# Kernel optimization log

Measured on AMD Instinct MI355X. Metric: run time of the kernel, lower is better.

Reference implementation:

```python
import jax, jax.numpy as jnp
import numpy as np

D_MODEL = 1024
NUM_HEADS = 16
B, S = 1, 4096


def setup_inputs() -> dict:
    key = jax.random.key(0)
    kx, kq, kk, kv, ko = jax.random.split(key, 5)
    std = (1.0 / D_MODEL) ** 0.5
    def trunc(k):
        return std * jax.random.truncated_normal(k, -3.0, 3.0, (D_MODEL, D_MODEL), dtype=jnp.float32)
    return {
        "x": jax.random.normal(kx, (B, S, D_MODEL), dtype=jnp.float32),
        "W_Q": trunc(kq),
        "W_K": trunc(kk),
        "W_V": trunc(kv),
        "W_O": trunc(ko),
    }


def reference(x, W_Q, W_K, W_V, W_O):
    Bx, Sx, Dm = x.shape
    H = NUM_HEADS
    d_attn = Dm // H
    # projections (torch code uses x @ W.T)
    Q = x @ W_Q.T
    K = x @ W_K.T
    V = x @ W_V.T
    # [B, H, S, d]
    Q = Q.reshape(Bx, Sx, H, d_attn).transpose(0, 2, 1, 3)
    K = K.reshape(Bx, Sx, H, d_attn).transpose(0, 2, 1, 3)
    V = V.reshape(Bx, Sx, H, d_attn).transpose(0, 2, 1, 3)
    scale = 1.0 / jnp.sqrt(jnp.asarray(d_attn, dtype=x.dtype))
    # [B, H, S, S] scores
    attn = jnp.einsum("bhqd,bhkd->bhqk", Q, K) * scale
    causal = jnp.tril(jnp.ones((Sx, Sx), dtype=bool))
    attn = jnp.where(causal, attn, jnp.asarray(-jnp.inf, dtype=attn.dtype))
    probs = jax.nn.softmax(attn, axis=-1)
    y = jnp.einsum("bhqk,bhkd->bhqd", probs, V)
    y = y.transpose(0, 2, 1, 3).reshape(Bx, Sx, Dm)
    return y @ W_O.T
```

## Files before the change

kernel.cpp:

```cpp
#include <hip/hip_runtime.h>

#define S_LEN 4096
#define DMODEL 1024
#define NHEADS 16

typedef __attribute__((ext_vector_type(8))) short bf16x8;
typedef __attribute__((ext_vector_type(4))) float f32x4;
typedef unsigned short u16;
typedef unsigned int u32;
typedef unsigned long long u64;

__device__ inline u16 f2bf(float f) {
    union { float f; u32 u; } v; v.f = f;
    u32 r = v.u + 0x7fffu + ((v.u >> 16) & 1u);
    return (u16)(r >> 16);
}

__device__ inline u32 pkbf2(float a, float b) {
    union { float f; u32 u; } ua, ub; ua.f = a; ub.f = b;
    const u32 ra = ua.u + 0x7fffu + ((ua.u >> 16) & 1u);
    const u32 rb = ub.u + 0x7fffu + ((ub.u >> 16) & 1u);
    return __builtin_amdgcn_perm(rb, ra, 0x07060302u);
}

__device__ inline u32 pkbf2f(float a, float b) {
    union { float f; u32 u; } ua, ub; ua.f = a; ub.f = b;
    const u32 ra = ua.u + 0x8000u;
    const u32 rb = ub.u + 0x8000u;
    return __builtin_amdgcn_perm(rb, ra, 0x07060302u);
}

__device__ inline void cp16(const void* g, void* l) {
    __builtin_amdgcn_global_load_lds(
        (const __attribute__((address_space(1))) unsigned int*)g,
        (__attribute__((address_space(3))) unsigned int*)l, 16, 0, 0);
}

__global__ __launch_bounds__(256) void cvt_all(const float* __restrict__ x,
                                               const float* __restrict__ wq,
                                               const float* __restrict__ wk,
                                               const float* __restrict__ wv,
                                               const float* __restrict__ wo,
                                               u16* __restrict__ xb,
                                               u16* __restrict__ w3,
                                               u16* __restrict__ wob) {
    const int b = blockIdx.x;
    const float* s; u16* d; int off;
    const int NW = DMODEL * DMODEL;
    if (b < 2048)      { s = x;  d = xb;          off = b * 2048; }
    else if (b < 2560) { s = wq; d = w3;          off = (b - 2048) * 2048; }
    else if (b < 3072) { s = wk; d = w3 + NW;     off = (b - 2560) * 2048; }
    else if (b < 3584) { s = wv; d = w3 + 2 * NW; off = (b - 3072) * 2048; }
    else               { s = wo; d = wob;         off = (b - 3584) * 2048; }
    const int i = off + threadIdx.x * 8;
    const float4 a = *(const float4*)(s + i);
    const float4 c = *(const float4*)(s + i + 4);
    u16 t[8];
    t[0] = f2bf(a.x); t[1] = f2bf(a.y); t[2] = f2bf(a.z); t[3] = f2bf(a.w);
    t[4] = f2bf(c.x); t[5] = f2bf(c.y); t[6] = f2bf(c.z); t[7] = f2bf(c.w);
    *(bf16x8*)(d + i) = *(const bf16x8*)t;
}

__global__ __launch_bounds__(256) void gemm_qkv(const u16* __restrict__ A,
                                                const u16* __restrict__ B3,
                                                u16* __restrict__ Qo,
                                                u16* __restrict__ Ko,
                                                u16* __restrict__ Vo) {
    __shared__ __align__(16) u16 As[2][128 * 32];
    __shared__ __align__(16) u16 Bs[2][128 * 32];
    const int tid = threadIdx.x, lane = tid & 63, wave = tid >> 6;
    const int wm = (wave >> 1) * 64, wn = (wave & 1) * 64;
    const int m0 = blockIdx.y * 128, n0 = blockIdx.x * 128;
    const int l15 = lane & 15, quad = lane >> 4;

    f32x4 acc[4][4];
#pragma unroll
    for (int i = 0; i < 4; i++)
#pragma unroll
        for (int j = 0; j < 4; j++) acc[i][j] = (f32x4){0.f, 0.f, 0.f, 0.f};

    const int r0 = tid >> 2, c0 = (tid & 3) * 8;

    cp16(A + (size_t)(m0 + r0) * 1024 + c0,       As[0] + r0 * 32 + c0);
    cp16(A + (size_t)(m0 + r0 + 64) * 1024 + c0,  As[0] + (r0 + 64) * 32 + c0);
    cp16(B3 + (size_t)(n0 + r0) * 1024 + c0,      Bs[0] + r0 * 32 + c0);
    cp16(B3 + (size_t)(n0 + r0 + 64) * 1024 + c0, Bs[0] + (r0 + 64) * 32 + c0);

    int cur = 0;
    for (int kk = 0; kk < 1024; kk += 32) {
        __syncthreads();
        if (kk + 32 < 1024) {
            const int kn = kk + 32;
            cp16(A + (size_t)(m0 + r0) * 1024 + kn + c0,       As[cur ^ 1] + r0 * 32 + c0);
            cp16(A + (size_t)(m0 + r0 + 64) * 1024 + kn + c0,  As[cur ^ 1] + (r0 + 64) * 32 + c0);
            cp16(B3 + (size_t)(n0 + r0) * 1024 + kn + c0,      Bs[cur ^ 1] + r0 * 32 + c0);
            cp16(B3 + (size_t)(n0 + r0 + 64) * 1024 + kn + c0, Bs[cur ^ 1] + (r0 + 64) * 32 + c0);
        }
        bf16x8 af[4], bfr[4];
#pragma unroll
        for (int i = 0; i < 4; i++)
            af[i] = *(const bf16x8*)(As[cur] + (wm + i * 16 + l15) * 32 + quad * 8);
#pragma unroll
        for (int j = 0; j < 4; j++)
            bfr[j] = *(const bf16x8*)(Bs[cur] + (wn + j * 16 + l15) * 32 + quad * 8);
#pragma unroll
        for (int i = 0; i < 4; i++)
#pragma unroll
            for (int j = 0; j < 4; j++)
                acc[i][j] = __builtin_amdgcn_mfma_f32_16x16x32_bf16(af[i], bfr[j], acc[i][j], 0, 0, 0);
        cur ^= 1;
    }

    const int which = n0 >> 10;
    const int n0r = n0 & 1023;
    u16* dst = (which == 0) ? Qo : (which == 1) ? Ko : Vo;
    const float sc = (which == 0) ? 0.125f * 1.4426950408889634f : 1.0f;
#pragma unroll
    for (int i = 0; i < 4; i++)
#pragma unroll
        for (int j = 0; j < 4; j++)
#pragma unroll
            for (int r = 0; r < 4; r++) {
                const int row = m0 + wm + i * 16 + quad * 4 + r;
                const int col = n0r + wn + j * 16 + l15;
                const int h = col >> 6, c = col & 63;
                const u16 v = f2bf(acc[i][j][r] * sc);
                if (which < 2) dst[(size_t)h * S_LEN * 64 + (size_t)row * 64 + c] = v;
                else           dst[(size_t)h * S_LEN * 64 + (size_t)c * S_LEN + row] = v;
            }
}

__global__ __launch_bounds__(256) void gemm_out(const u16* __restrict__ A,
                                                const u16* __restrict__ B,
                                                float* __restrict__ C) {
    __shared__ __align__(16) u16 As[2][64 * 64];
    __shared__ __align__(16) u16 Bs[2][128 * 64];
    const int tid = threadIdx.x, lane = tid & 63, wave = tid >> 6;
    const int wm = (wave >> 1) * 32, wn = (wave & 1) * 64;
    const int bx = blockIdx.x;
    const int n0 = (bx & 7) * 128, m0 = (bx >> 3) * 64;
    const int l15 = lane & 15, quad = lane >> 4;
    const int swz = l15 & 7;

    f32x4 acc[2][4];
#pragma unroll
    for (int i = 0; i < 2; i++)
#pragma unroll
        for (int j = 0; j < 4; j++) acc[i][j] = (f32x4){0.f, 0.f, 0.f, 0.f};

#define STAGE_OUT(buf, kb)                                                              \
    {                                                                                   \
        _Pragma("unroll")                                                               \
        for (int q = 0; q < 2; q++) {                                                   \
            const int ch = tid + q * 256;                                               \
            const int ar = ch >> 3, ac = ((ch & 7) ^ (ar & 7)) * 8;                     \
            cp16(A + (size_t)(m0 + ar) * 1024 + (kb) + ac, As[buf] + ch * 8);           \
        }                                                                               \
        _Pragma("unroll")                                                               \
        for (int q = 0; q < 4; q++) {                                                   \
            const int ch = tid + q * 256;                                               \
            const int br = ch >> 3, bc = ((ch & 7) ^ (br & 7)) * 8;                     \
            cp16(B + (size_t)(n0 + br) * 1024 + (kb) + bc, Bs[buf] + ch * 8);           \
        }                                                                               \
    }

    STAGE_OUT(0, 0);
    int cur = 0;
    for (int kk = 0; kk < 1024; kk += 64) {
        __syncthreads();
        if (kk + 64 < 1024) STAGE_OUT(cur ^ 1, kk + 64);
#pragma unroll
        for (int h = 0; h < 2; h++) {
            const int cc = (h * 4 + quad) ^ swz;
            bf16x8 af[2], bfr[4];
#pragma unroll
            for (int i = 0; i < 2; i++)
                af[i] = *(const bf16x8*)(As[cur] + (wm + i * 16 + l15) * 64 + cc * 8);
#pragma unroll
            for (int j = 0; j < 4; j++)
                bfr[j] = *(const bf16x8*)(Bs[cur] + (wn + j * 16 + l15) * 64 + cc * 8);
#pragma unroll
            for (int i = 0; i < 2; i++)
#pragma unroll
                for (int j = 0; j < 4; j++)
                    acc[i][j] = __builtin_amdgcn_mfma_f32_16x16x32_bf16(af[i], bfr[j], acc[i][j], 0, 0, 0);
        }
        cur ^= 1;
    }
#undef STAGE_OUT

#pragma unroll
    for (int i = 0; i < 2; i++)
#pragma unroll
        for (int j = 0; j < 4; j++)
#pragma unroll
            for (int r = 0; r < 4; r++) {
                const int row = m0 + wm + i * 16 + quad * 4 + r;
                const int col = n0 + wn + j * 16 + l15;
                C[(size_t)row * 1024 + col] = acc[i][j][r];
            }
}

__global__ __launch_bounds__(256) void attn(const u16* __restrict__ Q,
                                            const u16* __restrict__ Kh,
                                            const u16* __restrict__ Vt,
                                            u16* __restrict__ Y) {
    __shared__ __align__(16) u16 Ks[2][64 * 64];
    __shared__ __align__(16) u16 Vs[2][64 * 64];
    __shared__ __align__(16) u16 Pl[4][32 * 72];
    const int b = blockIdx.x;
    const int head = b & 15;
    const int bb = b >> 4;
    const int j = (b < 256) ? bb : 47 - bb;
    const int qaA = 64 * j;
    const int qaB = 64 * (63 - j);
    const int nktB = 64 - j;
    const int tid = threadIdx.x, lane = tid & 63, w = tid >> 6;
    const int l15 = lane & 15, quad = lane >> 4;
    const int swz = l15 & 7;

    const u16* Qp = Q + (size_t)head * S_LEN * 64;
    const u16* Kp = Kh + (size_t)head * S_LEN * 64;
    const u16* Vp = Vt + (size_t)head * 64 * S_LEN;

    const int qrowA = qaA + w * 16 + l15;
    const int qrowB = qaB + w * 16 + l15;
    const int srow = tid >> 3;
    const int scol = ((tid & 7) ^ (srow & 7)) * 8;

    bf16x8 aq[2][2];
#pragma unroll
    for (int s = 0; s < 2; s++) {
        aq[0][s] = *(const bf16x8*)(Qp + (size_t)qrowA * 64 + s * 32 + quad * 8);
        aq[1][s] = *(const bf16x8*)(Qp + (size_t)qrowB * 64 + s * 32 + quad * 8);
    }

    f32x4 o[2][4];
#pragma unroll
    for (int g = 0; g < 2; g++)
#pragma unroll
        for (int jj = 0; jj < 4; jj++) o[g][jj] = (f32x4){0.f, 0.f, 0.f, 0.f};
    float lrow[2] = {0.f, 0.f};

    cp16(Kp + (size_t)srow * 64 + scol,        Ks[0] + tid * 8);
    cp16(Kp + (size_t)(srow + 32) * 64 + scol, Ks[0] + tid * 8 + 2048);
    cp16(Vp + (size_t)srow * S_LEN + scol,        Vs[0] + tid * 8);
    cp16(Vp + (size_t)(srow + 32) * S_LEN + scol, Vs[0] + tid * 8 + 2048);

    int cur = 0;
    for (int kt = 0; kt < nktB; kt++) {
        __syncthreads();
        if (kt + 1 < nktB) {
            const int kn = (kt + 1) * 64;
            cp16(Kp + (size_t)(kn + srow) * 64 + scol,      Ks[cur ^ 1] + tid * 8);
            cp16(Kp + (size_t)(kn + srow + 32) * 64 + scol, Ks[cur ^ 1] + tid * 8 + 2048);
            cp16(Vp + (size_t)srow * S_LEN + kn + scol,        Vs[cur ^ 1] + tid * 8);
            cp16(Vp + (size_t)(srow + 32) * S_LEN + kn + scol, Vs[cur ^ 1] + tid * 8 + 2048);
        }
        const u16* K_ = Ks[cur];
        const u16* V_ = Vs[cur];
        const int kb = kt * 64;
        const bool actA = (kt <= j);
        const bool bndA = (kt == j);
        const bool bndB = (kt == nktB - 1);
#pragma unroll
        for (int t = 0; t < 4; t++) {
            const bf16x8 k0 = *(const bf16x8*)(K_ + (t * 16 + l15) * 64 + (quad ^ swz) * 8);
            const bf16x8 k1 = *(const bf16x8*)(K_ + (t * 16 + l15) * 64 + ((4 + quad) ^ swz) * 8);
            const int keyb = kb + t * 16 + quad * 4;
            {
                f32x4 c = (f32x4){0.f, 0.f, 0.f, 0.f};
                c = __builtin_amdgcn_mfma_f32_16x16x32_bf16(k0, aq[1][0], c, 0, 0, 0);
                c = __builtin_amdgcn_mfma_f32_16x16x32_bf16(k1, aq[1][1], c, 0, 0, 0);
                float p[4];
#pragma unroll
                for (int r = 0; r < 4; r++) {
                    p[r] = __builtin_amdgcn_exp2f(c[r]);
                    if (bndB && (keyb + r > qrowB)) p[r] = 0.f;
                }
                lrow[1] += (p[0] + p[1]) + (p[2] + p[3]);
                const u32 w0 = pkbf2f(p[0], p[1]);
                const u32 w1 = pkbf2f(p[2], p[3]);
                *(u64*)(&Pl[w][(16 + l15) * 72 + t * 16 + quad * 4]) =
                    (u64)w0 | ((u64)w1 << 32);
            }
            if (actA) {
                f32x4 c = (f32x4){0.f, 0.f, 0.f, 0.f};
                c = __builtin_amdgcn_mfma_f32_16x16x32_bf16(k0, aq[0][0], c, 0, 0, 0);
                c = __builtin_amdgcn_mfma_f32_16x16x32_bf16(k1, aq[0][1], c, 0, 0, 0);
                float p[4];
#pragma unroll
                for (int r = 0; r < 4; r++) {
                    p[r] = __builtin_amdgcn_exp2f(c[r]);
                    if (bndA && (keyb + r > qrowA)) p[r] = 0.f;
                }
                lrow[0] += (p[0] + p[1]) + (p[2] + p[3]);
                const u32 w0 = pkbf2f(p[0], p[1]);
                const u32 w1 = pkbf2f(p[2], p[3]);
                *(u64*)(&Pl[w][l15 * 72 + t * 16 + quad * 4]) =
                    (u64)w0 | ((u64)w1 << 32);
            }
        }
        bf16x8 pB0, pB1, pA0, pA1;
        pB0 = *(const bf16x8*)(&Pl[w][(16 + l15) * 72 + quad * 8]);
        pB1 = *(const bf16x8*)(&Pl[w][(16 + l15) * 72 + 32 + quad * 8]);
        if (actA) {
            pA0 = *(const bf16x8*)(&Pl[w][l15 * 72 + quad * 8]);
            pA1 = *(const bf16x8*)(&Pl[w][l15 * 72 + 32 + quad * 8]);
        }
#pragma unroll
        for (int jj = 0; jj < 4; jj++) {
            const bf16x8 v0 = *(const bf16x8*)(V_ + (jj * 16 + l15) * 64 + (quad ^ swz) * 8);
            const bf16x8 v1 = *(const bf16x8*)(V_ + (jj * 16 + l15) * 64 + ((4 + quad) ^ swz) * 8);
            o[1][jj] = __builtin_amdgcn_mfma_f32_16x16x32_bf16(v0, pB0, o[1][jj], 0, 0, 0);
            o[1][jj] = __builtin_amdgcn_mfma_f32_16x16x32_bf16(v1, pB1, o[1][jj], 0, 0, 0);
            if (actA) {
                o[0][jj] = __builtin_amdgcn_mfma_f32_16x16x32_bf16(v0, pA0, o[0][jj], 0, 0, 0);
                o[0][jj] = __builtin_amdgcn_mfma_f32_16x16x32_bf16(v1, pA1, o[0][jj], 0, 0, 0);
            }
        }
        cur ^= 1;
    }

#pragma unroll
    for (int g = 0; g < 2; g++) {
        lrow[g] += __shfl_xor(lrow[g], 16);
        lrow[g] += __shfl_xor(lrow[g], 32);
        const float inv = 1.f / lrow[g];
        const int qrow = (g == 0) ? qrowA : qrowB;
#pragma unroll
        for (int jj = 0; jj < 4; jj++) {
            const u32 w0 = pkbf2(o[g][jj][0] * inv, o[g][jj][1] * inv);
            const u32 w1 = pkbf2(o[g][jj][2] * inv, o[g][jj][3] * inv);
            *(u64*)(Y + (size_t)qrow * DMODEL + head * 64 + jj * 16 + quad * 4) =
                (u64)w0 | ((u64)w1 << 32);
        }
    }
}

extern "C" void kernel_launch(void* const* d_in, const int* in_sizes, int n_in,
                              void* d_out, int out_size, void* d_ws, size_t ws_size,
                              hipStream_t stream) {
    const float* x  = (const float*)d_in[0];
    const float* wq = (const float*)d_in[1];
    const float* wk = (const float*)d_in[2];
    const float* wv = (const float*)d_in[3];
    const float* wo = (const float*)d_in[4];
    float* out = (float*)d_out;

    u16* qh  = (u16*)d_ws;
    u16* kh  = qh + (size_t)S_LEN * DMODEL;
    u16* vt  = kh + (size_t)S_LEN * DMODEL;
    u16* xb  = vt + (size_t)S_LEN * DMODEL;
    u16* y   = xb;
    u16* wb3 = xb + (size_t)S_LEN * DMODEL;
    u16* wob = wb3 + (size_t)3 * DMODEL * DMODEL;

    const dim3 blk(256);

    cvt_all<<<4096, blk, 0, stream>>>(x, wq, wk, wv, wo, xb, wb3, wob);
    gemm_qkv<<<dim3(3 * DMODEL / 128, S_LEN / 128), blk, 0, stream>>>(xb, wb3, qh, kh, vt);
    attn<<<512, blk, 0, stream>>>(qh, kh, vt, y);
    gemm_out<<<512, blk, 0, stream>>>(y, wob, out);
}
```

Baseline: 221.1 us.

## Split attention keys across waves with one query tile per block and LDS reduction

The attention kernel now gives each block a single 64-row query tile (1024 blocks, longest tiles first) instead of pairing two tiles. Each wave takes a 16-key slice of every 128-key pair across all 64 queries, so P stays in registers rather than going through an LDS scratch buffer. Partial outputs and row sums are then reduced across the four waves through LDS at the end. This removes the P round-trip through LDS and doubles grid parallelism, at the cost of a cross-wave reduction epilogue, larger staging buffers and heavier register use (launch bounds of 2).

```diff
diff --git a/kernel.cpp b/kernel.cpp
--- a/kernel.cpp
+++ b/kernel.cpp
@@ -201,20 +201,18 @@
             }
 }
 
-__global__ __launch_bounds__(256) void attn(const u16* __restrict__ Q,
-                                            const u16* __restrict__ Kh,
-                                            const u16* __restrict__ Vt,
-                                            u16* __restrict__ Y) {
-    __shared__ __align__(16) u16 Ks[2][64 * 64];
-    __shared__ __align__(16) u16 Vs[2][64 * 64];
-    __shared__ __align__(16) u16 Pl[4][32 * 72];
+__global__ __launch_bounds__(256, 2) void attn(const u16* __restrict__ Q,
+                                               const u16* __restrict__ Kh,
+                                               const u16* __restrict__ Vt,
+                                               u16* __restrict__ Y) {
+    __shared__ __align__(16) u16 Ks[2][128 * 64];
+    __shared__ __align__(16) u16 Vs[2][64 * 128];
     const int b = blockIdx.x;
     const int head = b & 15;
-    const int bb = b >> 4;
-    const int j = (b < 256) ? bb : 47 - bb;
-    const int qaA = 64 * j;
-    const int qaB = 64 * (63 - j);
-    const int nktB = 64 - j;
+    const int jq = 63 - (b >> 4);
+    const int nkt = jq + 1;
+    const int np = (nkt + 1) >> 1;
+    const int qa = jq * 64;
     const int tid = threadIdx.x, lane = tid & 63, w = tid >> 6;
     const int l15 = lane & 15, quad = lane >> 4;
     const int swz = l15 & 7;
@@ -223,118 +221,157 @@
     const u16* Kp = Kh + (size_t)head * S_LEN * 64;
     const u16* Vp = Vt + (size_t)head * 64 * S_LEN;
 
-    const int qrowA = qaA + w * 16 + l15;
-    const int qrowB = qaB + w * 16 + l15;
-    const int srow = tid >> 3;
-    const int scol = ((tid & 7) ^ (srow & 7)) * 8;
-
-    bf16x8 aq[2][2];
-#pragma unroll
-    for (int s = 0; s < 2; s++) {
-        aq[0][s] = *(const bf16x8*)(Qp + (size_t)qrowA * 64 + s * 32 + quad * 8);
-        aq[1][s] = *(const bf16x8*)(Qp + (size_t)qrowB * 64 + s * 32 + quad * 8);
-    }
-
-    f32x4 o[2][4];
-#pragma unroll
-    for (int g = 0; g < 2; g++)
-#pragma unroll
-        for (int jj = 0; jj < 4; jj++) o[g][jj] = (f32x4){0.f, 0.f, 0.f, 0.f};
-    float lrow[2] = {0.f, 0.f};
-
-    cp16(Kp + (size_t)srow * 64 + scol,        Ks[0] + tid * 8);
-    cp16(Kp + (size_t)(srow + 32) * 64 + scol, Ks[0] + tid * 8 + 2048);
-    cp16(Vp + (size_t)srow * S_LEN + scol,        Vs[0] + tid * 8);
-    cp16(Vp + (size_t)(srow + 32) * S_LEN + scol, Vs[0] + tid * 8 + 2048);
-
+    bf16x8 qf[4][2];
+#pragma unroll
+    for (int qg = 0; qg < 4; qg++)
+#pragma unroll
+        for (int h = 0; h < 2; h++)
+            qf[qg][h] = *(const bf16x8*)(Qp + (size_t)(qa + qg * 16 + l15) * 64 + h * 32 + quad * 8);
+
+    f32x4 o[4][4];
+#pragma unroll
+    for (int dg = 0; dg < 4; dg++)
+#pragma unroll
+        for (int qg = 0; qg < 4; qg++) o[dg][qg] = (f32x4){0.f, 0.f, 0.f, 0.f};
+    float lp[4] = {0.f, 0.f, 0.f, 0.f};
+
+#define STAGE_PAIR(buf, kp2)                                                       \
+    {                                                                              \
+        _Pragma("unroll")                                                          \
+        for (int q = 0; q < 4; q++) {                                              \
+            const int ch = tid + q * 256;                                          \
+            const int kr = ch >> 3, kc = ((ch & 7) ^ (kr & 7)) * 8;                \
+            cp16(Kp + (size_t)((kp2) * 128 + kr) * 64 + kc, Ks[buf] + ch * 8);     \
+            const int vr = ch >> 4, lc = ch & 15;                                  \
+            const int vc = ((lc & 8) | ((lc & 7) ^ (vr & 7))) * 8;                 \
+            cp16(Vp + (size_t)vr * S_LEN + (kp2) * 128 + vc, Vs[buf] + ch * 8);    \
+        }                                                                          \
+    }
+
+    STAGE_PAIR(0, 0);
     int cur = 0;
-    for (int kt = 0; kt < nktB; kt++) {
+    for (int kp = 0; kp < np; kp++) {
         __syncthreads();
-        if (kt + 1 < nktB) {
-            const int kn = (kt + 1) * 64;
-            cp16(Kp + (size_t)(kn + srow) * 64 + scol,      Ks[cur ^ 1] + tid * 8);
-            cp16(Kp + (size_t)(kn + srow + 32) * 64 + scol, Ks[cur ^ 1] + tid * 8 + 2048);
-            cp16(Vp + (size_t)srow * S_LEN + kn + scol,        Vs[cur ^ 1] + tid * 8);
-            cp16(Vp + (size_t)(srow + 32) * S_LEN + kn + scol, Vs[cur ^ 1] + tid * 8 + 2048);
-        }
+        if (kp + 1 < np) STAGE_PAIR(cur ^ 1, kp + 1);
         const u16* K_ = Ks[cur];
         const u16* V_ = Vs[cur];
-        const int kb = kt * 64;
-        const bool actA = (kt <= j);
-        const bool bndA = (kt == j);
-        const bool bndB = (kt == nktB - 1);
-#pragma unroll
-        for (int t = 0; t < 4; t++) {
-            const bf16x8 k0 = *(const bf16x8*)(K_ + (t * 16 + l15) * 64 + (quad ^ swz) * 8);
-            const bf16x8 k1 = *(const bf16x8*)(K_ + (t * 16 + l15) * 64 + ((4 + quad) ^ swz) * 8);
-            const int keyb = kb + t * 16 + quad * 4;
-            {
-                f32x4 c = (f32x4){0.f, 0.f, 0.f, 0.f};
-                c = __builtin_amdgcn_mfma_f32_16x16x32_bf16(k0, aq[1][0], c, 0, 0, 0);
-                c = __builtin_amdgcn_mfma_f32_16x16x32_bf16(k1, aq[1][1], c, 0, 0, 0);
-                float p[4];
-#pragma unroll
-                for (int r = 0; r < 4; r++) {
-                    p[r] = __builtin_amdgcn_exp2f(c[r]);
-                    if (bndB && (keyb + r > qrowB)) p[r] = 0.f;
+        const bool hasO = (2 * kp + 1 < nkt);
+        const bool diagE = (2 * kp == jq);
+        const bool diagO = (2 * kp + 1 == jq);
+
+        const int rE = w * 16 + l15;
+        const bf16x8 kE0 = *(const bf16x8*)(K_ + rE * 64 + (quad ^ swz) * 8);
+        const bf16x8 kE1 = *(const bf16x8*)(K_ + rE * 64 + ((4 + quad) ^ swz) * 8);
+        bf16x8 kO0, kO1;
+        if (hasO) {
+            kO0 = *(const bf16x8*)(K_ + (rE + 64) * 64 + (quad ^ swz) * 8);
+            kO1 = *(const bf16x8*)(K_ + (rE + 64) * 64 + ((4 + quad) ^ swz) * 8);
+        }
+
+        const int keyl = w * 16 + quad * 4;
+        union { u32 d[4]; bf16x8 v; } pu[4];
+#pragma unroll
+        for (int qg = 0; qg < 4; qg++) {
+            const int ql = qg * 16 + l15;
+            f32x4 cE = (f32x4){0.f, 0.f, 0.f, 0.f};
+            cE = __builtin_amdgcn_mfma_f32_16x16x32_bf16(kE0, qf[qg][0], cE, 0, 0, 0);
+            cE = __builtin_amdgcn_mfma_f32_16x16x32_bf16(kE1, qf[qg][1], cE, 0, 0, 0);
+            float p0 = __builtin_amdgcn_exp2f(cE[0]);
+            float p1 = __builtin_amdgcn_exp2f(cE[1]);
+            float p2 = __builtin_amdgcn_exp2f(cE[2]);
+            float p3 = __builtin_amdgcn_exp2f(cE[3]);
+            if (diagE) {
+                if (keyl + 0 > ql) p0 = 0.f;
+                if (keyl + 1 > ql) p1 = 0.f;
+                if (keyl + 2 > ql) p2 = 0.f;
+                if (keyl + 3 > ql) p3 = 0.f;
+            }
+            lp[qg] += (p0 + p1) + (p2 + p3);
+            pu[qg].d[0] = pkbf2f(p0, p1);
+            pu[qg].d[1] = pkbf2f(p2, p3);
+            if (hasO) {
+                f32x4 cO = (f32x4){0.f, 0.f, 0.f, 0.f};
+                cO = __builtin_amdgcn_mfma_f32_16x16x32_bf16(kO0, qf[qg][0], cO, 0, 0, 0);
+                cO = __builtin_amdgcn_mfma_f32_16x16x32_bf16(kO1, qf[qg][1], cO, 0, 0, 0);
+                float q0 = __builtin_amdgcn_exp2f(cO[0]);
+                float q1 = __builtin_amdgcn_exp2f(cO[1]);
+                float q2 = __builtin_amdgcn_exp2f(cO[2]);
+                float q3 = __builtin_amdgcn_exp2f(cO[3]);
+                if (diagO) {
+                    if (keyl + 0 > ql) q0 = 0.f;
+                    if (keyl + 1 > ql) q1 = 0.f;
+                    if (keyl + 2 > ql) q2 = 0.f;
+                    if (keyl + 3 > ql) q3 = 0.f;
                 }
-                lrow[1] += (p[0] + p[1]) + (p[2] + p[3]);
-                const u32 w0 = pkbf2f(p[0], p[1]);
-                const u32 w1 = pkbf2f(p[2], p[3]);
-                *(u64*)(&Pl[w][(16 + l15) * 72 + t * 16 + quad * 4]) =
-                    (u64)w0 | ((u64)w1 << 32);
+                lp[qg] += (q0 + q1) + (q2 + q3);
+                pu[qg].d[2] = pkbf2f(q0, q1);
+                pu[qg].d[3] = pkbf2f(q2, q3);
+            } else {
+                pu[qg].d[2] = 0u;
+                pu[qg].d[3] = 0u;
             }
-            if (actA) {
-                f32x4 c = (f32x4){0.f, 0.f, 0.f, 0.f};
-                c = __builtin_amdgcn_mfma_f32_16x16x32_bf16(k0, aq[0][0], c, 0, 0, 0);
-                c = __builtin_amdgcn_mfma_f32_16x16x32_bf16(k1, aq[0][1], c, 0, 0, 0);
-                float p[4];
-#pragma unroll
-                for (int r = 0; r < 4; r++) {
-                    p[r] = __builtin_amdgcn_exp2f(c[r]);
-                    if (bndA && (keyb + r > qrowA)) p[r] = 0.f;
-                }
-                lrow[0] += (p[0] + p[1]) + (p[2] + p[3]);
-                const u32 w0 = pkbf2f(p[0], p[1]);
-                const u32 w1 = pkbf2f(p[2], p[3]);
-                *(u64*)(&Pl[w][l15 * 72 + t * 16 + quad * 4]) =
-                    (u64)w0 | ((u64)w1 << 32);
-            }
-        }
-        bf16x8 pB0, pB1, pA0, pA1;
-        pB0 = *(const bf16x8*)(&Pl[w][(16 + l15) * 72 + quad * 8]);
-        pB1 = *(const bf16x8*)(&Pl[w][(16 + l15) * 72 + 32 + quad * 8]);
-        if (actA) {
-            pA0 = *(const bf16x8*)(&Pl[w][l15 * 72 + quad * 8]);
-            pA1 = *(const bf16x8*)(&Pl[w][l15 * 72 + 32 + quad * 8]);
-        }
-#pragma unroll
-        for (int jj = 0; jj < 4; jj++) {
-            const bf16x8 v0 = *(const bf16x8*)(V_ + (jj * 16 + l15) * 64 + (quad ^ swz) * 8);
-            const bf16x8 v1 = *(const bf16x8*)(V_ + (jj * 16 + l15) * 64 + ((4 + quad) ^ swz) * 8);
-            o[1][jj] = __builtin_amdgcn_mfma_f32_16x16x32_bf16(v0, pB0, o[1][jj], 0, 0, 0);
-            o[1][jj] = __builtin_amdgcn_mfma_f32_16x16x32_bf16(v1, pB1, o[1][jj], 0, 0, 0);
-            if (actA) {
-                o[0][jj] = __builtin_amdgcn_mfma_f32_16x16x32_bf16(v0, pA0, o[0][jj], 0, 0, 0);
-                o[0][jj] = __builtin_amdgcn_mfma_f32_16x16x32_bf16(v1, pA1, o[0][jj], 0, 0, 0);
-            }
+        }
+
+#pragma unroll
+        for (int dg = 0; dg < 4; dg++) {
+            const int vrow = dg * 16 + l15;
+            const int gcE = w * 2 + (quad >> 1);
+            const int sc = gcE ^ swz;
+            union { u64 d[2]; bf16x8 v; } vf;
+            vf.d[0] = *(const u64*)(V_ + vrow * 128 + sc * 8 + (quad & 1) * 4);
+            vf.d[1] = hasO ? *(const u64*)(V_ + vrow * 128 + (8 | sc) * 8 + (quad & 1) * 4)
+                           : 0ull;
+#pragma unroll
+            for (int qg = 0; qg < 4; qg++)
+                o[dg][qg] = __builtin_amdgcn_mfma_f32_16x16x32_bf16(vf.v, pu[qg].v, o[dg][qg], 0, 0, 0);
         }
         cur ^= 1;
     }
-
-#pragma unroll
-    for (int g = 0; g < 2; g++) {
-        lrow[g] += __shfl_xor(lrow[g], 16);
-        lrow[g] += __shfl_xor(lrow[g], 32);
-        const float inv = 1.f / lrow[g];
-        const int qrow = (g == 0) ? qrowA : qrowB;
-#pragma unroll
-        for (int jj = 0; jj < 4; jj++) {
-            const u32 w0 = pkbf2(o[g][jj][0] * inv, o[g][jj][1] * inv);
-            const u32 w1 = pkbf2(o[g][jj][2] * inv, o[g][jj][3] * inv);
-            *(u64*)(Y + (size_t)qrow * DMODEL + head * 64 + jj * 16 + quad * 4) =
-                (u64)w0 | ((u64)w1 << 32);
-        }
+#undef STAGE_PAIR
+
+#pragma unroll
+    for (int qg = 0; qg < 4; qg++) {
+        lp[qg] += __shfl_xor(lp[qg], 16);
+        lp[qg] += __shfl_xor(lp[qg], 32);
+    }
+    __syncthreads();
+    float* OR = (float*)&Ks[0][0];
+    float* LR = (float*)&Vs[0][0];
+    if (lane < 16) {
+#pragma unroll
+        for (int qg = 0; qg < 4; qg++) LR[(w * 4 + qg) * 16 + lane] = lp[qg];
+    }
+#pragma unroll
+    for (int c = 0; c < 2; c++) {
+        if (c) __syncthreads();
+#pragma unroll
+        for (int d2 = 0; d2 < 2; d2++)
+#pragma unroll
+            for (int qg = 0; qg < 4; qg++)
+                *(f32x4*)&OR[(((w * 2 + d2) * 4 + qg) * 16 + l15) * 16 + quad * 4] = o[c * 2 + d2][qg];
+        __syncthreads();
+        const int d2r = w >> 1, qh = w & 1;
+        const int qrow = qh * 32 + (lane >> 1);
+        const int qg = qrow >> 4, lq = qrow & 15;
+        const int dd = (lane & 1) * 8;
+        f32x4 sa = (f32x4){0.f, 0.f, 0.f, 0.f};
+        f32x4 sb = (f32x4){0.f, 0.f, 0.f, 0.f};
+#pragma unroll
+        for (int sw = 0; sw < 4; sw++) {
+            const float* p = &OR[(((sw * 2 + d2r) * 4 + qg) * 16 + lq) * 16 + dd];
+            sa += *(const f32x4*)p;
+            sb += *(const f32x4*)(p + 4);
+        }
+        const float l = LR[qg * 16 + lq] + LR[(4 + qg) * 16 + lq] +
+                        LR[(8 + qg) * 16 + lq] + LR[(12 + qg) * 16 + lq];
+        const float inv = 1.f / l;
+        const int dg = c * 2 + d2r;
+        union { u32 d[4]; bf16x8 v; } yv;
+        yv.d[0] = pkbf2(sa[0] * inv, sa[1] * inv);
+        yv.d[1] = pkbf2(sa[2] * inv, sa[3] * inv);
+        yv.d[2] = pkbf2(sb[0] * inv, sb[1] * inv);
+        yv.d[3] = pkbf2(sb[2] * inv, sb[3] * inv);
+        *(bf16x8*)(Y + (size_t)(qa + qrow) * DMODEL + head * 64 + dg * 16 + dd) = yv.v;
     }
 }
 
@@ -360,6 +397,6 @@
 
     cvt_all<<<4096, blk, 0, stream>>>(x, wq, wk, wv, wo, xb, wb3, wob);
     gemm_qkv<<<dim3(3 * DMODEL / 128, S_LEN / 128), blk, 0, stream>>>(xb, wb3, qh, kh, vt);
-    attn<<<512, blk, 0, stream>>>(qh, kh, vt, y);
+    attn<<<1024, blk, 0, stream>>>(qh, kh, vt, y);
     gemm_out<<<512, blk, 0, stream>>>(y, wob, out);
 }
```

Result: faster. 206.5 us (-6.6%).
